# Performance work log

Measured on AMD Instinct MI355X. Metric: run time of the kernel, lower is better.

## Reference

```python
import jax, jax.numpy as jnp
import numpy as np

N, D_FEAT, D, H, L = 2048, 128, 256, 8, 2
DH = D // H
E = 65536
NUM_EDGE_TYPES = 8
MAX_DIST = 10
MAX_DEGREE = 512
D_FF = 4 * D
D_OUT = 128
EPS = 1e-5


def _layernorm(x, g, b):
    mu = jnp.mean(x, axis=-1, keepdims=True)
    var = jnp.mean(jnp.square(x - mu), axis=-1, keepdims=True)
    return (x - mu) * jax.lax.rsqrt(var + EPS) * g + b


def setup_inputs() -> dict:
    key = jax.random.key(0)
    ks = jax.random.split(key, 32)
    inp = {
        "x": jax.random.normal(ks[0], (N, D_FEAT), dtype=jnp.float32),
        "edge_index": jax.random.randint(ks[1], (2, E), 0, N),
        "edge_types": jax.random.randint(ks[2], (E,), 0, NUM_EDGE_TYPES),
        "pos_encoding": jax.random.uniform(ks[3], (N, N), dtype=jnp.float32),
    }
    def xavier(k, shape):
        fan_in, fan_out = shape[0], shape[1]
        lim = float(np.sqrt(6.0 / (fan_in + fan_out)))
        return jax.random.uniform(k, shape, jnp.float32, -lim, lim)
    inp["W_emb"] = xavier(ks[4], (D_FEAT, D)); inp["b_emb"] = jnp.zeros((D,), jnp.float32)
    # stacked per-layer params, stored as [in, out] so y = x @ W + b
    inp["Wq"] = jnp.stack([xavier(jax.random.fold_in(ks[5], l), (D, D)) for l in range(L)])
    inp["Wk"] = jnp.stack([xavier(jax.random.fold_in(ks[6], l), (D, D)) for l in range(L)])
    inp["Wv"] = jnp.stack([xavier(jax.random.fold_in(ks[7], l), (D, D)) for l in range(L)])
    inp["Wo"] = jnp.stack([xavier(jax.random.fold_in(ks[8], l), (D, D)) for l in range(L)])
    for nm in ("bq", "bk", "bv", "bo"):
        inp[nm] = jnp.zeros((L, D), jnp.float32)
    inp["spd_table"] = 0.02 * jax.random.normal(ks[9], (L, MAX_DIST + 1, H), dtype=jnp.float32)
    inp["edge_table"] = 0.02 * jax.random.normal(ks[10], (L, NUM_EDGE_TYPES, H), dtype=jnp.float32)
    inp["din_emb"] = 0.02 * jax.random.normal(ks[11], (L, MAX_DEGREE + 1, D), dtype=jnp.float32)
    inp["dout_emb"] = 0.02 * jax.random.normal(ks[12], (L, MAX_DEGREE + 1, D), dtype=jnp.float32)
    inp["ln1_g"] = jnp.ones((L, D), jnp.float32); inp["ln1_b"] = jnp.zeros((L, D), jnp.float32)
    inp["ln2_g"] = jnp.ones((L, D), jnp.float32); inp["ln2_b"] = jnp.zeros((L, D), jnp.float32)
    inp["W1"] = jnp.stack([xavier(jax.random.fold_in(ks[13], l), (D, D_FF)) for l in range(L)])
    inp["b1"] = jnp.zeros((L, D_FF), jnp.float32)
    inp["W2"] = jnp.stack([xavier(jax.random.fold_in(ks[14], l), (D_FF, D)) for l in range(L)])
    inp["b2"] = jnp.zeros((L, D), jnp.float32)
    inp["W_out"] = xavier(ks[15], (D, D_OUT)); inp["b_out"] = jnp.zeros((D_OUT,), jnp.float32)
    return inp


def _forward(x, edge_index, edge_types, pos_encoding,
             W_emb, b_emb, Wq, bq, Wk, bk, Wv, bv, Wo, bo,
             spd_table, edge_table, din_emb, dout_emb,
             ln1_g, ln1_b, ln2_g, ln2_b, W1, b1, W2, b2, W_out, b_out):
    src, dst = edge_index[0], edge_index[1]
    ones = jnp.ones((E,), jnp.int32)
    deg_out = jnp.clip(jax.ops.segment_sum(ones, src, num_segments=N), 0, MAX_DEGREE)
    deg_in = jnp.clip(jax.ops.segment_sum(ones, dst, num_segments=N), 0, MAX_DEGREE)
    # SPD bucket matrix [N, N] (int), shared across layers
    spd_bucket = jnp.clip(pos_encoding[:, :N] * MAX_DIST + 0.5, 0, MAX_DIST).astype(jnp.int32)

    h = x @ W_emb + b_emb  # node embedding; dropout=0 (eval)
    scale = 1.0 / np.sqrt(DH)
    for l in range(L):
        # centrality encoding
        h = h + din_emb[l][deg_in] + dout_emb[l][deg_out]
        xn = _layernorm(h, ln1_g[l], ln1_b[l])
        q = (xn @ Wq[l] + bq[l]).reshape(N, H, DH).transpose(1, 0, 2)  # [H,N,DH]
        k = (xn @ Wk[l] + bk[l]).reshape(N, H, DH).transpose(1, 0, 2)
        v = (xn @ Wv[l] + bv[l]).reshape(N, H, DH).transpose(1, 0, 2)
        # attention bias [H, N, N]: SPD table gather + per-edge scatter-add
        bias = spd_table[l][spd_bucket].transpose(2, 0, 1)
        e_bias = edge_table[l][edge_types]  # [E, H]
        bias = bias.at[:, src, dst].add(e_bias.T)
        scores = jnp.einsum('hnd,hmd->hnm', q, k) * scale + bias
        attn = jax.nn.softmax(scores, axis=-1)
        attn_out = jnp.einsum('hnm,hmd->hnd', attn, v).transpose(1, 0, 2).reshape(N, D)
        h = h + attn_out @ Wo[l] + bo[l]
        y = _layernorm(h, ln2_g[l], ln2_b[l])
        y = jax.nn.gelu(y @ W1[l] + b1[l], approximate=False) @ W2[l] + b2[l]
        h = h + y
    return h @ W_out + b_out


def reference(x, edge_index, edge_types, pos_encoding,
              W_emb, b_emb, Wq, bq, Wk, bk, Wv, bv, Wo, bo,
              spd_table, edge_table, din_emb, dout_emb,
              ln1_g, ln1_b, ln2_g, ln2_b, W1, b1, W2, b2, W_out, b_out):
    return _forward(x, edge_index, edge_types, pos_encoding,
                    W_emb, b_emb, Wq, bq, Wk, bk, Wv, bv, Wo, bo,
                    spd_table, edge_table, din_emb, dout_emb,
                    ln1_g, ln1_b, ln2_g, ln2_b, W1, b1, W2, b2, W_out, b_out)
```

## Files before the change

### kernel.cpp

```cpp
#include <hip/hip_runtime.h>
#include <math.h>

#define N_NODES 2048
#define D_MODEL 256
#define D_FEAT 128
#define NHEAD 8
#define DH 32
#define NLAYER 2
#define NEDGE 65536
#define D_FF 1024
#define D_OUT 128
#define MAXDEG 512
#define JSPLIT 4

typedef __attribute__((ext_vector_type(8))) short short8;
typedef __attribute__((ext_vector_type(4))) float f32x4;
typedef __attribute__((ext_vector_type(4))) unsigned short u16x4;

__device__ __forceinline__ unsigned short f2bf(float f) {
    unsigned u = __float_as_uint(f);
    unsigned r = (u + 0x7FFFu + ((u >> 16) & 1u)) >> 16;
    return (unsigned short)r;
}

template <int CTRL>
__device__ __forceinline__ float dpp_ror(float x) {
    return __int_as_float(__builtin_amdgcn_update_dpp(0, __float_as_int(x), CTRL, 0xf, 0xf, false));
}

__device__ __forceinline__ void wt_tile(const float* __restrict__ W, unsigned short* __restrict__ Wt,
                                        int K, int Nc, int n0, int k0, int tid,
                                        unsigned short (*tile)[33]) {
    int r = tid >> 3, cg = (tid & 7) * 4;
    float4 w4 = *(const float4*)&W[(size_t)(k0 + r) * Nc + n0 + cg];
    tile[r][cg + 0] = f2bf(w4.x); tile[r][cg + 1] = f2bf(w4.y);
    tile[r][cg + 2] = f2bf(w4.z); tile[r][cg + 3] = f2bf(w4.w);
    __syncthreads();
    int c = tid >> 3, rg = (tid & 7) * 4;
    u16x4 o;
    #pragma unroll
    for (int j = 0; j < 4; j++) o[j] = tile[rg + j][c];
    *(u16x4*)&Wt[(size_t)(n0 + c) * K + k0 + rg] = o;
}

__global__ void mega_prep_kernel(const float* __restrict__ pos, unsigned char* __restrict__ bucket,
                                 unsigned* __restrict__ hist, int* __restrict__ deg_out,
                                 int* __restrict__ deg_in, unsigned* __restrict__ gcursor,
                                 const float* __restrict__ Wq, const float* __restrict__ Wk,
                                 const float* __restrict__ Wv, const float* __restrict__ Wo,
                                 const float* __restrict__ W1, const float* __restrict__ W2,
                                 const float* __restrict__ W_emb, const float* __restrict__ W_out,
                                 const float* __restrict__ bq, const float* __restrict__ bk,
                                 const float* __restrict__ bv,
                                 unsigned short* __restrict__ qkvt, unsigned short* __restrict__ wot,
                                 unsigned short* __restrict__ w1t, unsigned short* __restrict__ w2t,
                                 unsigned short* __restrict__ wembt, unsigned short* __restrict__ woutt,
                                 float* __restrict__ bqkv) {
    __shared__ unsigned short tile[32][33];
    int b = blockIdx.x, tid = threadIdx.x;
    if (b < 4096) {
        int i = b * 256 + tid;
        float4 p = *(const float4*)&pos[(size_t)i * 4];
        unsigned b0 = (unsigned)fminf(fmaxf(p.x * 10.f + 0.5f, 0.f), 10.f);
        unsigned b1 = (unsigned)fminf(fmaxf(p.y * 10.f + 0.5f, 0.f), 10.f);
        unsigned b2 = (unsigned)fminf(fmaxf(p.z * 10.f + 0.5f, 0.f), 10.f);
        unsigned b3 = (unsigned)fminf(fmaxf(p.w * 10.f + 0.5f, 0.f), 10.f);
        ((unsigned*)bucket)[i] = b0 | (b1 << 8) | (b2 << 16) | (b3 << 24);
        if (b < 64) {
            #pragma unroll
            for (int k = 0; k < 4; k++) hist[b * 1024 + k * 256 + tid] = 0;
        } else if (b == 64) {
            #pragma unroll
            for (int k = 0; k < 8; k++) deg_out[k * 256 + tid] = 0;
            #pragma unroll
            for (int k = 0; k < 8; k++) deg_in[k * 256 + tid] = 0;
            if (tid == 0) *gcursor = 0;
        }
        return;
    }
    int bb = b - 4096;
    if (bb < 512) {
        int z = bb >> 6, t = bb & 63;
        int l = z >> 2, which = z & 3;
        const float* W = (which == 0 ? Wq : which == 1 ? Wk : which == 2 ? Wv : Wo) + (size_t)l * 65536;
        unsigned short* dst = (which < 3) ? qkvt + (size_t)l * 196608 + which * 65536
                                          : wot + (size_t)l * 65536;
        wt_tile(W, dst, 256, 256, (t & 7) * 32, (t >> 3) * 32, tid, tile);
    } else if (bb < 1024) {
        int b2 = bb - 512, l = b2 >> 8, t = b2 & 255;
        wt_tile(W1 + (size_t)l * D_MODEL * D_FF, w1t + (size_t)l * D_MODEL * D_FF,
                D_MODEL, D_FF, (t & 31) * 32, (t >> 5) * 32, tid, tile);
    } else if (bb < 1536) {
        int b3 = bb - 1024, l = b3 >> 8, t = b3 & 255;
        wt_tile(W2 + (size_t)l * D_FF * D_MODEL, w2t + (size_t)l * D_FF * D_MODEL,
                D_FF, D_MODEL, (t & 7) * 32, (t >> 3) * 32, tid, tile);
    } else if (bb < 1568) {
        int b4 = bb - 1536;
        wt_tile(W_emb, wembt, D_FEAT, D_MODEL, (b4 & 7) * 32, (b4 >> 3) * 32, tid, tile);
    } else if (bb < 1600) {
        int b5 = bb - 1568;
        wt_tile(W_out, woutt, D_MODEL, D_OUT, (b5 & 3) * 32, (b5 >> 2) * 32, tid, tile);
    } else {
        int i = (bb - 1600) * 256 + tid;
        if (i < NLAYER * 768) {
            int l = i / 768, j = i % 768;
            const float* src = j < 256 ? bq : j < 512 ? bk : bv;
            bqkv[i] = src[l * 256 + (j & 255)];
        }
    }
}

__global__ void degree_hist_kernel(const int* __restrict__ ei,
                                   int* __restrict__ deg_out, int* __restrict__ deg_in,
                                   unsigned* __restrict__ hist) {
    int e = blockIdx.x * 256 + threadIdx.x;
    if (e < NEDGE) {
        int src = ei[e], dst = ei[NEDGE + e];
        atomicAdd(&deg_out[src], 1);
        atomicAdd(&deg_in[dst], 1);
        atomicAdd(&hist[(src >> 6) * 2048 + dst], 1);
    }
}

__global__ void edge_alloc_kernel(const unsigned* __restrict__ hist,
                                  unsigned* __restrict__ offsets, unsigned* __restrict__ cursor,
                                  unsigned* __restrict__ gend, unsigned* __restrict__ gcursor) {
    int g = blockIdx.x;
    int t = threadIdx.x;
    unsigned v = hist[g * 64 + t];
    unsigned inc = v;
    #pragma unroll
    for (int off = 1; off < 64; off <<= 1) {
        unsigned u = __shfl_up(inc, off);
        if (t >= off) inc += u;
    }
    unsigned total = __shfl(inc, 63);
    unsigned base = 0;
    if (t == 63) base = atomicAdd(gcursor, total);
    base = __shfl(base, 63);
    unsigned o = base + inc - v;
    offsets[g * 64 + t] = o;
    cursor[g * 64 + t] = o;
    if (t == 63) gend[g] = base + total;
}

__global__ void edge_scatter_kernel(const int* __restrict__ ei, const int* __restrict__ etypes,
                                    unsigned* __restrict__ cursor, unsigned* __restrict__ packed) {
    int e = blockIdx.x * 256 + threadIdx.x;
    if (e < NEDGE) {
        int src = ei[e], dst = ei[NEDGE + e];
        int key = (src >> 6) * 2048 + dst;
        unsigned pos = atomicAdd(&cursor[key], 1);
        packed[pos] = (unsigned)dst | ((unsigned)(src & 63) << 11) | ((unsigned)etypes[e] << 17);
    }
}

__global__ void centrality_ln_kernel(float* __restrict__ h,
                                     const float* __restrict__ din_l,
                                     const float* __restrict__ dout_l,
                                     const int* __restrict__ deg_in,
                                     const int* __restrict__ deg_out,
                                     const float* __restrict__ g,
                                     const float* __restrict__ b,
                                     unsigned short* __restrict__ y) {
    int row = blockIdx.x;
    int tid = threadIdx.x;
    int di = min(max(deg_in[row], 0), MAXDEG);
    int dn = min(max(deg_out[row], 0), MAXDEG);
    float v = h[row * D_MODEL + tid] + din_l[di * D_MODEL + tid] + dout_l[dn * D_MODEL + tid];
    h[row * D_MODEL + tid] = v;
    __shared__ float red[256];
    red[tid] = v; __syncthreads();
    for (int s = 128; s > 0; s >>= 1) { if (tid < s) red[tid] += red[tid + s]; __syncthreads(); }
    float mu = red[0] * (1.0f / D_MODEL);
    __syncthreads();
    float d = v - mu;
    red[tid] = d * d; __syncthreads();
    for (int s = 128; s > 0; s >>= 1) { if (tid < s) red[tid] += red[tid + s]; __syncthreads(); }
    float rstd = rsqrtf(red[0] * (1.0f / D_MODEL) + 1e-5f);
    y[row * D_MODEL + tid] = f2bf(d * rstd * g[tid] + b[tid]);
}

__global__ void layernorm_kernel(const float* __restrict__ x,
                                 const float* __restrict__ g,
                                 const float* __restrict__ b,
                                 unsigned short* __restrict__ y) {
    int row = blockIdx.x;
    int tid = threadIdx.x;
    float v = x[row * D_MODEL + tid];
    __shared__ float red[256];
    red[tid] = v; __syncthreads();
    for (int s = 128; s > 0; s >>= 1) { if (tid < s) red[tid] += red[tid + s]; __syncthreads(); }
    float mu = red[0] * (1.0f / D_MODEL);
    __syncthreads();
    float d = v - mu;
    red[tid] = d * d; __syncthreads();
    for (int s = 128; s > 0; s >>= 1) { if (tid < s) red[tid] += red[tid + s]; __syncthreads(); }
    float rstd = rsqrtf(red[0] * (1.0f / D_MODEL) + 1e-5f);
    y[row * D_MODEL + tid] = f2bf(d * rstd * g[tid] + b[tid]);
}

template <int ACT, bool RESID, bool OUTBF16, bool AFP32>
__global__ void gemm_mfma_kernel(const void* __restrict__ Av,
                                 const unsigned short* __restrict__ Wt,
                                 const float* __restrict__ bias,
                                 float* __restrict__ C, unsigned short* __restrict__ Cb,
                                 int Nc, int K) {
    __shared__ __align__(16) unsigned short As[32][72];
    __shared__ __align__(16) unsigned short Bs[64][72];
    const unsigned short* A16 = (const unsigned short*)Av;
    const float* A32 = (const float*)Av;
    int tid = threadIdx.x;
    int m0 = blockIdx.y * 32, n0 = blockIdx.x * 64;
    int w = tid >> 6, lane = tid & 63;
    int rg = (w & 1) * 16, cg = (w >> 1) * 32;
    int m = lane & 15, quad = lane >> 4;
    f32x4 acc[2] = {{0.f, 0.f, 0.f, 0.f}, {0.f, 0.f, 0.f, 0.f}};
    int ar = tid >> 3, ac = (tid & 7) * 8;
    uint4 ra; float4 fa0, fa1; uint4 rb0, rb1;
    if (AFP32) {
        fa0 = *(const float4*)&A32[(size_t)(m0 + ar) * K + ac];
        fa1 = *(const float4*)&A32[(size_t)(m0 + ar) * K + ac + 4];
    } else {
        ra = *(const uint4*)&A16[(size_t)(m0 + ar) * K + ac];
    }
    rb0 = *(const uint4*)&Wt[(size_t)(n0 + ar) * K + ac];
    rb1 = *(const uint4*)&Wt[(size_t)(n0 + 32 + ar) * K + ac];
    for (int k0 = 0; k0 < K; k0 += 64) {
        if (AFP32) {
            u16x4 t0 = {f2bf(fa0.x), f2bf(fa0.y), f2bf(fa0.z), f2bf(fa0.w)};
            u16x4 t1 = {f2bf(fa1.x), f2bf(fa1.y), f2bf(fa1.z), f2bf(fa1.w)};
            *(u16x4*)&As[ar][ac] = t0;
            *(u16x4*)&As[ar][ac + 4] = t1;
        } else {
            *(uint4*)&As[ar][ac] = ra;
        }
        *(uint4*)&Bs[ar][ac] = rb0;
        *(uint4*)&Bs[ar + 32][ac] = rb1;
        __syncthreads();
        int kn = k0 + 64;
        if (kn < K) {
            if (AFP32) {
                fa0 = *(const float4*)&A32[(size_t)(m0 + ar) * K + kn + ac];
                fa1 = *(const float4*)&A32[(size_t)(m0 + ar) * K + kn + ac + 4];
            } else {
                ra = *(const uint4*)&A16[(size_t)(m0 + ar) * K + kn + ac];
            }
            rb0 = *(const uint4*)&Wt[(size_t)(n0 + ar) * K + kn + ac];
            rb1 = *(const uint4*)&Wt[(size_t)(n0 + 32 + ar) * K + kn + ac];
        }
        #pragma unroll
        for (int ks = 0; ks < 2; ks++) {
            short8 a = *(const short8*)&As[rg + m][ks * 32 + quad * 8];
            #pragma unroll
            for (int t = 0; t < 2; t++) {
                short8 b = *(const short8*)&Bs[cg + t * 16 + m][ks * 32 + quad * 8];
                acc[t] = __builtin_amdgcn_mfma_f32_16x16x32_bf16(a, b, acc[t], 0, 0, 0);
            }
        }
        __syncthreads();
    }
    #pragma unroll
    for (int t = 0; t < 2; t++) {
        #pragma unroll
        for (int reg = 0; reg < 4; reg++) {
            int row = m0 + rg + quad * 4 + reg;
            int col = n0 + cg + t * 16 + m;
            float val = acc[t][reg] + bias[col];
            if (ACT == 1) val = val * 0.5f * (1.0f + erff(val * 0.7071067811865476f));
            size_t idx = (size_t)row * Nc + col;
            if (RESID) val += C[idx];
            if (OUTBF16) Cb[idx] = f2bf(val);
            else C[idx] = val;
        }
    }
}

__global__ void gemm_qkv_kernel(const unsigned short* __restrict__ A,
                                const unsigned short* __restrict__ Wt,
                                const float* __restrict__ bias,
                                unsigned short* __restrict__ Cb,
                                unsigned short* __restrict__ vbt) {
    const int K = D_MODEL, Nc = 768;
    __shared__ __align__(16) unsigned short As[32][72];
    __shared__ __align__(16) unsigned short Bs[64][72];
    int tid = threadIdx.x;
    int m0 = blockIdx.y * 32, n0 = blockIdx.x * 64;
    int w = tid >> 6, lane = tid & 63;
    int rg = (w & 1) * 16, cg = (w >> 1) * 32;
    int m = lane & 15, quad = lane >> 4;
    f32x4 acc[2] = {{0.f, 0.f, 0.f, 0.f}, {0.f, 0.f, 0.f, 0.f}};
    int ar = tid >> 3, ac = (tid & 7) * 8;
    uint4 ra = *(const uint4*)&A[(size_t)(m0 + ar) * K + ac];
    uint4 rb0 = *(const uint4*)&Wt[(size_t)(n0 + ar) * K + ac];
    uint4 rb1 = *(const uint4*)&Wt[(size_t)(n0 + 32 + ar) * K + ac];
    for (int k0 = 0; k0 < K; k0 += 64) {
        *(uint4*)&As[ar][ac] = ra;
        *(uint4*)&Bs[ar][ac] = rb0;
        *(uint4*)&Bs[ar + 32][ac] = rb1;
        __syncthreads();
        int kn = k0 + 64;
        if (kn < K) {
            ra = *(const uint4*)&A[(size_t)(m0 + ar) * K + kn + ac];
            rb0 = *(const uint4*)&Wt[(size_t)(n0 + ar) * K + kn + ac];
            rb1 = *(const uint4*)&Wt[(size_t)(n0 + 32 + ar) * K + kn + ac];
        }
        #pragma unroll
        for (int ks = 0; ks < 2; ks++) {
            short8 a = *(const short8*)&As[rg + m][ks * 32 + quad * 8];
            #pragma unroll
            for (int t = 0; t < 2; t++) {
                short8 b = *(const short8*)&Bs[cg + t * 16 + m][ks * 32 + quad * 8];
                acc[t] = __builtin_amdgcn_mfma_f32_16x16x32_bf16(a, b, acc[t], 0, 0, 0);
            }
        }
        __syncthreads();
    }
    if (n0 >= 512) {
        #pragma unroll
        for (int t = 0; t < 2; t++) {
            int cl = cg + t * 16 + m;
            float bcol = bias[n0 + cl];
            u16x4 tv;
            #pragma unroll
            for (int reg = 0; reg < 4; reg++) tv[reg] = f2bf(acc[t][reg] + bcol);
            *(u16x4*)&Bs[cl][rg + quad * 4] = tv;
        }
        __syncthreads();
        int rr = tid >> 2, cc = (tid & 3) * 8;
        uint4 o0 = *(const uint4*)&Bs[rr][cc];
        *(uint4*)&vbt[(size_t)(n0 - 512 + rr) * N_NODES + m0 + cc] = o0;
        return;
    }
    #pragma unroll
    for (int t = 0; t < 2; t++) {
        #pragma unroll
        for (int reg = 0; reg < 4; reg++) {
            int row = m0 + rg + quad * 4 + reg;
            int col = n0 + cg + t * 16 + m;
            Cb[(size_t)row * Nc + col] = f2bf(acc[t][reg] + bias[col]);
        }
    }
}

__global__ void gemm_oproj_kernel(const float* __restrict__ part_O,
                                  const float* __restrict__ l_part,
                                  const unsigned short* __restrict__ Wt,
                                  const float* __restrict__ bias,
                                  float* __restrict__ C) {
    __shared__ __align__(16) unsigned short As[32][72];
    __shared__ __align__(16) unsigned short Bs[64][72];
    int tid = threadIdx.x;
    int m0 = blockIdx.y * 32, n0 = blockIdx.x * 64;
    int w = tid >> 6, lane = tid & 63;
    int rg = (w & 1) * 16, cg = (w >> 1) * 32;
    int m = lane & 15, quad = lane >> 4;
    f32x4 acc[2] = {{0.f, 0.f, 0.f, 0.f}, {0.f, 0.f, 0.f, 0.f}};
    int ar = tid >> 3, ac = (tid & 7) * 8;
    int row = m0 + ar;
    for (int k0 = 0; k0 < D_MODEL; k0 += 64) {
        int col = k0 + ac;
        int hh = col >> 5;
        float L = 0.f;
        float o[8] = {0.f, 0.f, 0.f, 0.f, 0.f, 0.f, 0.f, 0.f};
        #pragma unroll
        for (int js = 0; js < JSPLIT; js++) {
            L += l_part[((size_t)js * NHEAD + hh) * N_NODES + row];
            const float* pp = &part_O[((size_t)js * N_NODES + row) * D_MODEL + col];
            float4 p0 = *(const float4*)pp;
            float4 p1 = *(const float4*)(pp + 4);
            o[0] += p0.x; o[1] += p0.y; o[2] += p0.z; o[3] += p0.w;
            o[4] += p1.x; o[5] += p1.y; o[6] += p1.z; o[7] += p1.w;
        }
        float inv = 1.0f / L;
        u16x4 t0, t1;
        #pragma unroll
        for (int j = 0; j < 4; j++) { t0[j] = f2bf(o[j] * inv); t1[j] = f2bf(o[j + 4] * inv); }
        *(u16x4*)&As[ar][ac] = t0;
        *(u16x4*)&As[ar][ac + 4] = t1;
        *(uint4*)&Bs[ar][ac] = *(const uint4*)&Wt[(size_t)(n0 + ar) * D_MODEL + k0 + ac];
        *(uint4*)&Bs[ar + 32][ac] = *(const uint4*)&Wt[(size_t)(n0 + 32 + ar) * D_MODEL + k0 + ac];
        __syncthreads();
        #pragma unroll
        for (int ks = 0; ks < 2; ks++) {
            short8 a = *(const short8*)&As[rg + m][ks * 32 + quad * 8];
            #pragma unroll
            for (int t = 0; t < 2; t++) {
                short8 b = *(const short8*)&Bs[cg + t * 16 + m][ks * 32 + quad * 8];
                acc[t] = __builtin_amdgcn_mfma_f32_16x16x32_bf16(a, b, acc[t], 0, 0, 0);
            }
        }
        __syncthreads();
    }
    #pragma unroll
    for (int t = 0; t < 2; t++) {
        #pragma unroll
        for (int reg = 0; reg < 4; reg++) {
            int orow = m0 + rg + quad * 4 + reg;
            int ocol = n0 + cg + t * 16 + m;
            size_t idx = (size_t)orow * D_MODEL + ocol;
            C[idx] += acc[t][reg] + bias[ocol];
        }
    }
}

__global__ __launch_bounds__(256)
void flash_attn_kernel(const unsigned short* __restrict__ qkvb,
                       const unsigned short* __restrict__ vbt,
                       const unsigned char* __restrict__ bucket,
                       const float* __restrict__ spd_l,
                       const float* __restrict__ et_l,
                       const unsigned* __restrict__ offsets,
                       const unsigned* __restrict__ gend,
                       const unsigned* __restrict__ packed,
                       float* __restrict__ part_O,
                       float* __restrict__ l_part) {
    __shared__ __align__(16) unsigned short ks[2][64][40];
    __shared__ __align__(16) unsigned short vs[2][32][72];
    __shared__ __align__(16) float ov[64][68];
    __shared__ float et[8];

    int tid = threadIdx.x;
    int rb = blockIdx.x;
    int i0 = rb * 64;
    int hh = blockIdx.y;
    int js = blockIdx.z;
    int lane = tid & 63;
    if (tid < 8) et[tid] = et_l[tid * NHEAD + hh];
    float spd_reg = spd_l[(lane < 11 ? lane : 10) * NHEAD + hh];

    int w = tid >> 6;
    int m = lane & 15, quad = lane >> 4;
    int r0 = w * 16;
    short8 aq = *(const short8*)&qkvb[(size_t)(i0 + r0 + m) * 768 + hh * DH + quad * 8];
    float l_st[4] = {0.f, 0.f, 0.f, 0.f};
    f32x4 oacc[2] = {{0.f, 0.f, 0.f, 0.f}, {0.f, 0.f, 0.f, 0.f}};
    const float scale = 0.17677669529663687f;
    const int NT = N_NODES / JSPLIT / 64;

    int krow = tid >> 2, kcol = (tid & 3) * 8;
    int vrow = tid >> 3, vcol = (tid & 7) * 8;
    int erow = r0 + (lane >> 2);
    int ecol = (lane & 3) * 16;

    int jbase = js * (N_NODES / JSPLIT);
    uint4 kpre = *(const uint4*)&qkvb[(size_t)(jbase + krow) * 768 + 256 + hh * DH + kcol];
    uint4 vpre = *(const uint4*)&vbt[(size_t)(hh * DH + vrow) * N_NODES + jbase + vcol];
    uint4 bpre = *(const uint4*)&bucket[(size_t)(i0 + erow) * N_NODES + jbase + ecol];
    *(uint4*)&ks[0][krow][kcol] = kpre;
    *(uint4*)&vs[0][vrow][vcol] = vpre;
    {
        const unsigned char* bb = (const unsigned char*)&bpre;
        #pragma unroll
        for (int g = 0; g < 4; g++) {
            f32x4 st;
            #pragma unroll
            for (int i2 = 0; i2 < 4; i2++)
                st[i2] = __int_as_float(__builtin_amdgcn_ds_bpermute(
                    ((int)bb[g * 4 + i2]) << 2, __float_as_int(spd_reg)));
            *(f32x4*)&ov[erow][ecol + g * 4] = st;
        }
    }

    int buf = 0;
    for (int jt = 0; jt < NT; jt++) {
        int j0 = jbase + jt * 64;
        __syncthreads();
        {
            unsigned key0 = (unsigned)rb * 2048 + j0;
            unsigned start = offsets[key0], end = gend[key0 >> 6];
            for (unsigned i = start + tid; i < end; i += 256) {
                unsigned p = packed[i];
                atomicAdd(&ov[(p >> 11) & 63][(p & 2047) - j0], et[(p >> 17) & 7]);
            }
        }
        if (jt + 1 < NT) {
            int jn = j0 + 64;
            kpre = *(const uint4*)&qkvb[(size_t)(jn + krow) * 768 + 256 + hh * DH + kcol];
            vpre = *(const uint4*)&vbt[(size_t)(hh * DH + vrow) * N_NODES + jn + vcol];
            bpre = *(const uint4*)&bucket[(size_t)(i0 + erow) * N_NODES + jn + ecol];
        }
        __syncthreads();
        float sv[4][4];
        #pragma unroll
        for (int t = 0; t < 4; t++) {
            short8 bk8 = *(const short8*)&ks[buf][t * 16 + m][quad * 8];
            f32x4 z = {0.f, 0.f, 0.f, 0.f};
            f32x4 sacc = __builtin_amdgcn_mfma_f32_16x16x32_bf16(aq, bk8, z, 0, 0, 0);
            #pragma unroll
            for (int r = 0; r < 4; r++)
                sv[t][r] = __expf(sacc[r] * scale + ov[r0 + quad * 4 + r][t * 16 + m]);
        }
        #pragma unroll
        for (int r = 0; r < 4; r++) {
            float ps = sv[0][r] + sv[1][r] + sv[2][r] + sv[3][r];
            ps += dpp_ror<0x121>(ps);
            ps += dpp_ror<0x122>(ps);
            ps += dpp_ror<0x124>(ps);
            ps += dpp_ror<0x128>(ps);
            l_st[r] += ps;
        }
        #pragma unroll
        for (int t = 0; t < 4; t++)
            #pragma unroll
            for (int r = 0; r < 4; r++)
                ov[r0 + quad * 4 + r][t * 16 + m] = sv[t][r];
        __builtin_amdgcn_s_waitcnt(0xC07F);
        #pragma unroll
        for (int kh = 0; kh < 2; kh++) {
            f32x4 p0 = *(const f32x4*)&ov[r0 + m][kh * 32 + quad * 8];
            f32x4 p1 = *(const f32x4*)&ov[r0 + m][kh * 32 + quad * 8 + 4];
            short8 pa;
            pa[0] = (short)f2bf(p0[0]); pa[1] = (short)f2bf(p0[1]);
            pa[2] = (short)f2bf(p0[2]); pa[3] = (short)f2bf(p0[3]);
            pa[4] = (short)f2bf(p1[0]); pa[5] = (short)f2bf(p1[1]);
            pa[6] = (short)f2bf(p1[2]); pa[7] = (short)f2bf(p1[3]);
            #pragma unroll
            for (int t = 0; t < 2; t++) {
                short8 vb = *(const short8*)&vs[buf][t * 16 + m][kh * 32 + quad * 8];
                oacc[t] = __builtin_amdgcn_mfma_f32_16x16x32_bf16(pa, vb, oacc[t], 0, 0, 0);
            }
        }
        if (jt + 1 < NT) {
            *(uint4*)&ks[buf ^ 1][krow][kcol] = kpre;
            *(uint4*)&vs[buf ^ 1][vrow][vcol] = vpre;
            const unsigned char* bb = (const unsigned char*)&bpre;
            #pragma unroll
            for (int g = 0; g < 4; g++) {
                f32x4 st;
                #pragma unroll
                for (int i2 = 0; i2 < 4; i2++)
                    st[i2] = __int_as_float(__builtin_amdgcn_ds_bpermute(
                        ((int)bb[g * 4 + i2]) << 2, __float_as_int(spd_reg)));
                *(f32x4*)&ov[erow][ecol + g * 4] = st;
            }
            buf ^= 1;
        }
    }
    #pragma unroll
    for (int t = 0; t < 2; t++)
        #pragma unroll
        for (int r = 0; r < 4; r++)
            part_O[((size_t)js * N_NODES + i0 + r0 + quad * 4 + r) * D_MODEL + hh * DH + t * 16 + m] =
                oacc[t][r];
    if (m == 0) {
        #pragma unroll
        for (int r = 0; r < 4; r++) {
            int row = i0 + r0 + quad * 4 + r;
            l_part[((size_t)js * NHEAD + hh) * N_NODES + row] = l_st[r];
        }
    }
}

#define WS_ALLOC(type, name, count) \
    type* name = (type*)base; base += (((size_t)(count) * sizeof(type)) + 255) & ~(size_t)255;

extern "C" void kernel_launch(void* const* d_in, const int* in_sizes, int n_in,
                              void* d_out, int out_size, void* d_ws, size_t ws_size,
                              hipStream_t stream) {
    const float* x          = (const float*)d_in[0];
    const int*   edge_index = (const int*)d_in[1];
    const int*   edge_types = (const int*)d_in[2];
    const float* pos        = (const float*)d_in[3];
    const float* W_emb      = (const float*)d_in[4];
    const float* b_emb      = (const float*)d_in[5];
    const float* Wq         = (const float*)d_in[6];
    const float* Wk         = (const float*)d_in[7];
    const float* Wv         = (const float*)d_in[8];
    const float* Wo         = (const float*)d_in[9];
    const float* bq         = (const float*)d_in[10];
    const float* bk         = (const float*)d_in[11];
    const float* bv         = (const float*)d_in[12];
    const float* bo         = (const float*)d_in[13];
    const float* spd_table  = (const float*)d_in[14];
    const float* edge_table = (const float*)d_in[15];
    const float* din_emb    = (const float*)d_in[16];
    const float* dout_emb   = (const float*)d_in[17];
    const float* ln1_g      = (const float*)d_in[18];
    const float* ln1_b      = (const float*)d_in[19];
    const float* ln2_g      = (const float*)d_in[20];
    const float* ln2_b      = (const float*)d_in[21];
    const float* W1         = (const float*)d_in[22];
    const float* b1         = (const float*)d_in[23];
    const float* W2         = (const float*)d_in[24];
    const float* b2         = (const float*)d_in[25];
    const float* W_out      = (const float*)d_in[26];
    const float* b_out      = (const float*)d_in[27];
    float* out = (float*)d_out;

    char* base = (char*)d_ws;
    WS_ALLOC(int, deg_out, N_NODES)
    WS_ALLOC(int, deg_in, N_NODES)
    WS_ALLOC(float, h, N_NODES * D_MODEL)
    WS_ALLOC(unsigned short, xb, N_NODES * D_MODEL)
    WS_ALLOC(unsigned short, qkvb, N_NODES * 768)
    WS_ALLOC(unsigned short, vbt, D_MODEL * N_NODES)
    WS_ALLOC(unsigned short, ffnb, N_NODES * D_FF)
    WS_ALLOC(unsigned char, bucket, (size_t)N_NODES * N_NODES)
    WS_ALLOC(unsigned short, qkvt, NLAYER * 768 * D_MODEL)
    WS_ALLOC(unsigned short, wot, NLAYER * D_MODEL * D_MODEL)
    WS_ALLOC(unsigned short, w1t, NLAYER * D_MODEL * D_FF)
    WS_ALLOC(unsigned short, w2t, NLAYER * D_FF * D_MODEL)
    WS_ALLOC(unsigned short, wembt, D_FEAT * D_MODEL)
    WS_ALLOC(unsigned short, woutt, D_MODEL * D_OUT)
    WS_ALLOC(float, bqkv, NLAYER * 768)
    WS_ALLOC(unsigned, hist, 65536)
    WS_ALLOC(unsigned, offsets, 65536)
    WS_ALLOC(unsigned, cursor, 65536)
    WS_ALLOC(unsigned, gend, 1024)
    WS_ALLOC(unsigned, gcursor, 1)
    WS_ALLOC(unsigned, packed, NEDGE)
    WS_ALLOC(float, part_O, (size_t)JSPLIT * N_NODES * D_MODEL)
    WS_ALLOC(float, l_part, (size_t)JSPLIT * NHEAD * N_NODES)

    mega_prep_kernel<<<5702, 256, 0, stream>>>(pos, bucket, hist, deg_out, deg_in, gcursor,
                                               Wq, Wk, Wv, Wo, W1, W2, W_emb, W_out,
                                               bq, bk, bv, qkvt, wot, w1t, w2t, wembt, woutt, bqkv);
    degree_hist_kernel<<<NEDGE / 256, 256, 0, stream>>>(edge_index, deg_out, deg_in, hist);
    edge_alloc_kernel<<<1024, 64, 0, stream>>>(hist, offsets, cursor, gend, gcursor);
    edge_scatter_kernel<<<NEDGE / 256, 256, 0, stream>>>(edge_index, edge_types, cursor, packed);

    gemm_mfma_kernel<0, false, false, true><<<dim3(D_MODEL / 64, N_NODES / 32), 256, 0, stream>>>(
        x, wembt, b_emb, h, nullptr, D_MODEL, D_FEAT);

    for (int l = 0; l < NLAYER; l++) {
        centrality_ln_kernel<<<N_NODES, 256, 0, stream>>>(
            h, din_emb + (size_t)l * (MAXDEG + 1) * D_MODEL,
            dout_emb + (size_t)l * (MAXDEG + 1) * D_MODEL, deg_in, deg_out,
            ln1_g + l * D_MODEL, ln1_b + l * D_MODEL, xb);

        gemm_qkv_kernel<<<dim3(768 / 64, N_NODES / 32), 256, 0, stream>>>(
            xb, qkvt + (size_t)l * 768 * D_MODEL, bqkv + l * 768, qkvb, vbt);

        flash_attn_kernel<<<dim3(N_NODES / 64, NHEAD, JSPLIT), 256, 0, stream>>>(
            qkvb, vbt, bucket, spd_table + (size_t)l * 11 * NHEAD,
            edge_table + (size_t)l * 8 * NHEAD, offsets, gend, packed, part_O, l_part);

        gemm_oproj_kernel<<<dim3(D_MODEL / 64, N_NODES / 32), 256, 0, stream>>>(
            part_O, l_part, wot + (size_t)l * D_MODEL * D_MODEL, bo + l * D_MODEL, h);

        layernorm_kernel<<<N_NODES, 256, 0, stream>>>(h, ln2_g + l * D_MODEL, ln2_b + l * D_MODEL, xb);

        gemm_mfma_kernel<1, false, true, false><<<dim3(D_FF / 64, N_NODES / 32), 256, 0, stream>>>(
            xb, w1t + (size_t)l * D_MODEL * D_FF, b1 + l * D_FF, nullptr, ffnb, D_FF, D_MODEL);

        gemm_mfma_kernel<0, true, false, false><<<dim3(D_MODEL / 64, N_NODES / 32), 256, 0, stream>>>(
            ffnb, w2t + (size_t)l * D_FF * D_MODEL, b2 + l * D_MODEL, h, nullptr, D_MODEL, D_FF);
    }

    gemm_mfma_kernel<0, false, false, true><<<dim3(D_OUT / 64, N_NODES / 32), 256, 0, stream>>>(
        h, woutt, b_out, out, nullptr, D_OUT, D_MODEL);
}
```

Measured before the change: 300.3 us.

## Transpose score MFMA, store probabilities as packed bf16 in swizzled LDS

The QK^T MFMA operands are swapped so each lane holds a row's consecutive score columns. This lets each lane read its bias as one vector load, keep a per-lane row-sum, and skip the per-tile DPP cross-lane reductions, which are replaced by two bpermutes at the end. Probabilities are converted to bf16 once and written packed into the shared tile, so the PV stage reads ready-made MFMA operands instead of converting floats. An XOR swizzle on LDS columns is added to avoid bank conflicts, at the cost of extra index arithmetic in the edge scatter atomics.

```diff
diff --git a/kernel.cpp b/kernel.cpp
--- a/kernel.cpp
+++ b/kernel.cpp
@@ -21,11 +21,6 @@
     unsigned u = __float_as_uint(f);
     unsigned r = (u + 0x7FFFu + ((u >> 16) & 1u)) >> 16;
     return (unsigned short)r;
-}
-
-template <int CTRL>
-__device__ __forceinline__ float dpp_ror(float x) {
-    return __int_as_float(__builtin_amdgcn_update_dpp(0, __float_as_int(x), CTRL, 0xf, 0xf, false));
 }
 
 __device__ __forceinline__ void wt_tile(const float* __restrict__ W, unsigned short* __restrict__ Wt,
@@ -433,7 +428,7 @@
     int m = lane & 15, quad = lane >> 4;
     int r0 = w * 16;
     short8 aq = *(const short8*)&qkvb[(size_t)(i0 + r0 + m) * 768 + hh * DH + quad * 8];
-    float l_st[4] = {0.f, 0.f, 0.f, 0.f};
+    float l_acc = 0.f;
     f32x4 oacc[2] = {{0.f, 0.f, 0.f, 0.f}, {0.f, 0.f, 0.f, 0.f}};
     const float scale = 0.17677669529663687f;
     const int NT = N_NODES / JSPLIT / 64;
@@ -442,6 +437,8 @@
     int vrow = tid >> 3, vcol = (tid & 7) * 8;
     int erow = r0 + (lane >> 2);
     int ecol = (lane & 3) * 16;
+    int eswz = (erow & 7) << 2;
+    int cswz = (m & 7) << 2;
 
     int jbase = js * (N_NODES / JSPLIT);
     uint4 kpre = *(const uint4*)&qkvb[(size_t)(jbase + krow) * 768 + 256 + hh * DH + kcol];
@@ -458,7 +455,7 @@
             for (int i2 = 0; i2 < 4; i2++)
                 st[i2] = __int_as_float(__builtin_amdgcn_ds_bpermute(
                     ((int)bb[g * 4 + i2]) << 2, __float_as_int(spd_reg)));
-            *(f32x4*)&ov[erow][ecol + g * 4] = st;
+            *(f32x4*)&ov[erow][(ecol + g * 4) ^ eswz] = st;
         }
     }
 
@@ -471,7 +468,9 @@
             unsigned start = offsets[key0], end = gend[key0 >> 6];
             for (unsigned i = start + tid; i < end; i += 256) {
                 unsigned p = packed[i];
-                atomicAdd(&ov[(p >> 11) & 63][(p & 2047) - j0], et[(p >> 17) & 7]);
+                int arow = (p >> 11) & 63;
+                int acol = ((p & 2047) - j0) ^ ((arow & 7) << 2);
+                atomicAdd(&ov[arow][acol], et[(p >> 17) & 7]);
             }
         }
         if (jt + 1 < NT) {
@@ -486,35 +485,30 @@
         for (int t = 0; t < 4; t++) {
             short8 bk8 = *(const short8*)&ks[buf][t * 16 + m][quad * 8];
             f32x4 z = {0.f, 0.f, 0.f, 0.f};
-            f32x4 sacc = __builtin_amdgcn_mfma_f32_16x16x32_bf16(aq, bk8, z, 0, 0, 0);
-            #pragma unroll
-            for (int r = 0; r < 4; r++)
-                sv[t][r] = __expf(sacc[r] * scale + ov[r0 + quad * 4 + r][t * 16 + m]);
-        }
-        #pragma unroll
-        for (int r = 0; r < 4; r++) {
-            float ps = sv[0][r] + sv[1][r] + sv[2][r] + sv[3][r];
-            ps += dpp_ror<0x121>(ps);
-            ps += dpp_ror<0x122>(ps);
-            ps += dpp_ror<0x124>(ps);
-            ps += dpp_ror<0x128>(ps);
-            l_st[r] += ps;
-        }
-        #pragma unroll
-        for (int t = 0; t < 4; t++)
-            #pragma unroll
-            for (int r = 0; r < 4; r++)
-                ov[r0 + quad * 4 + r][t * 16 + m] = sv[t][r];
+            f32x4 sacc = __builtin_amdgcn_mfma_f32_16x16x32_bf16(bk8, aq, z, 0, 0, 0);
+            f32x4 bv = *(const f32x4*)&ov[r0 + m][(t * 16 + quad * 4) ^ cswz];
+            #pragma unroll
+            for (int r = 0; r < 4; r++) {
+                float pv = __expf(sacc[r] * scale + bv[r]);
+                sv[t][r] = pv;
+                l_acc += pv;
+            }
+        }
+        unsigned* ovrow = (unsigned*)&ov[r0 + m][0];
+        #pragma unroll
+        for (int t = 0; t < 4; t++) {
+            #pragma unroll
+            for (int rp = 0; rp < 2; rp++) {
+                unsigned d = (unsigned)f2bf(sv[t][2 * rp]) |
+                             ((unsigned)f2bf(sv[t][2 * rp + 1]) << 16);
+                ovrow[(8 * t + 2 * quad + rp) ^ cswz] = d;
+            }
+        }
         __builtin_amdgcn_s_waitcnt(0xC07F);
         #pragma unroll
         for (int kh = 0; kh < 2; kh++) {
-            f32x4 p0 = *(const f32x4*)&ov[r0 + m][kh * 32 + quad * 8];
-            f32x4 p1 = *(const f32x4*)&ov[r0 + m][kh * 32 + quad * 8 + 4];
-            short8 pa;
-            pa[0] = (short)f2bf(p0[0]); pa[1] = (short)f2bf(p0[1]);
-            pa[2] = (short)f2bf(p0[2]); pa[3] = (short)f2bf(p0[3]);
-            pa[4] = (short)f2bf(p1[0]); pa[5] = (short)f2bf(p1[1]);
-            pa[6] = (short)f2bf(p1[2]); pa[7] = (short)f2bf(p1[3]);
+            uint4 pd = *(const uint4*)&ovrow[(16 * kh + 4 * quad) ^ cswz];
+            short8 pa = *(short8*)&pd;
             #pragma unroll
             for (int t = 0; t < 2; t++) {
                 short8 vb = *(const short8*)&vs[buf][t * 16 + m][kh * 32 + quad * 8];
@@ -532,7 +526,7 @@
                 for (int i2 = 0; i2 < 4; i2++)
                     st[i2] = __int_as_float(__builtin_amdgcn_ds_bpermute(
                         ((int)bb[g * 4 + i2]) << 2, __float_as_int(spd_reg)));
-                *(f32x4*)&ov[erow][ecol + g * 4] = st;
+                *(f32x4*)&ov[erow][(ecol + g * 4) ^ eswz] = st;
             }
             buf ^= 1;
         }
@@ -543,13 +537,10 @@
         for (int r = 0; r < 4; r++)
             part_O[((size_t)js * N_NODES + i0 + r0 + quad * 4 + r) * D_MODEL + hh * DH + t * 16 + m] =
                 oacc[t][r];
-    if (m == 0) {
-        #pragma unroll
-        for (int r = 0; r < 4; r++) {
-            int row = i0 + r0 + quad * 4 + r;
-            l_part[((size_t)js * NHEAD + hh) * N_NODES + row] = l_st[r];
-        }
-    }
+    l_acc += __int_as_float(__builtin_amdgcn_ds_bpermute((lane ^ 16) << 2, __float_as_int(l_acc)));
+    l_acc += __int_as_float(__builtin_amdgcn_ds_bpermute((lane ^ 32) << 2, __float_as_int(l_acc)));
+    if (quad == 0)
+        l_part[((size_t)js * NHEAD + hh) * N_NODES + i0 + r0 + m] = l_acc;
 }
 
 #define WS_ALLOC(type, name, count) \
```

Result: slower. 317.3 us (+5.6%).
